# Performance work log

Measured on AMD Instinct MI355X. Metric: run time of the kernel, lower is better.

The kernel has to match this reference:

```python
import jax, jax.numpy as jnp
import numpy as np

ITEMNUM = 50000
NUM_HEADS = 4
EPS = 1e-8


def _ln(x, g, b):
    m = x.mean(-1, keepdims=True)
    v = ((x - m) ** 2).mean(-1, keepdims=True)
    return (x - m) * jax.lax.rsqrt(v + EPS) * g + b


def _forward(seqs_data, position, seqs, time_emb, pos_table, gate_W, gate_b,
             ln_attn_g, ln_attn_b, qW, qb, kW, kb, vW, vb,
             ln_ffn_g, ln_ffn_b, c1W, c1b, c2W, c2b, last_g, last_b):
    B, L, H = seqs.shape
    nb = qW.shape[0]
    hd = H // NUM_HEADS

    pe = pos_table[position]                      # [B,L,H]
    seqs = seqs + pe
    time = time_emb + pe
    # per-position per-block time gates, [B,L,nb]
    gates = jax.nn.sigmoid(jnp.einsum('blh,nh->bln', time, gate_W) + gate_b)

    keep = (seqs_data != ITEMNUM - 1)[..., None].astype(seqs.dtype)  # [B,L,1]
    seqs = seqs * keep
    tril = jnp.tril(jnp.ones((L, L), dtype=bool))  # causal: keep lower triangle
    neg_inf = jnp.asarray(-jnp.inf, seqs.dtype)
    scale = 1.0 / np.sqrt(hd).astype(np.float32)

    for i in range(nb):
        Q = _ln(seqs, ln_attn_g[i], ln_attn_b[i])
        q = Q @ qW[i].T + qb[i]
        k = time @ kW[i].T + kb[i]
        v = (seqs + time) @ vW[i].T + vb[i]
        # [B,nh,L,hd]
        q = q.reshape(B, L, NUM_HEADS, hd).transpose(0, 2, 1, 3)
        k = k.reshape(B, L, NUM_HEADS, hd).transpose(0, 2, 1, 3)
        v = v.reshape(B, L, NUM_HEADS, hd).transpose(0, 2, 1, 3)
        scores = jnp.einsum('bhqd,bhkd->bhqk', q, k) * scale  # [B,nh,L,L]
        tg = gates[:, :, i]                                   # [B,L]
        gate_mat = tg[:, None, :, None] * tg[:, None, None, :]  # [B,1,L,L] outer product
        scores = jnp.where(tril[None, None], scores * gate_mat, neg_inf)
        attn = jax.nn.softmax(scores, axis=-1)
        out = jnp.einsum('bhqk,bhkd->bhqd', attn, v)
        out = out.transpose(0, 2, 1, 3).reshape(B, L, H)
        x = Q + out
        x = _ln(x, ln_ffn_g[i], ln_ffn_b[i])
        # PointWiseFeedForward: two 1x1 convs == two linears, relu, residual
        h = jax.nn.relu(x @ c1W[i].T + c1b[i])
        seqs = (h @ c2W[i].T + c2b[i] + x) * keep

    return _ln(seqs, last_g, last_b)


def setup_inputs() -> dict:
    key = jax.random.key(0)
    B, L, H, NB, ML = 64, 512, 256, 2, 512
    ks = iter(jax.random.split(key, 32))
    nrm = lambda shape, s=0.05: jax.random.normal(next(ks), shape, jnp.float32) * s
    pos_table = nrm((ML, H), 0.02).at[0].set(0.0)  # padding_idx=0
    inp = {
        'seqs_data': jax.random.randint(next(ks), (B, L), 0, ITEMNUM - 1, jnp.int32),
        'seqs': nrm((B, L, H), 1.0),
        'position': jax.random.randint(next(ks), (B, L), 0, ML, jnp.int32),
        'time_emb': nrm((B, L, H), 1.0),
        'pos_table': pos_table,
        'gate_W': nrm((NB, H)), 'gate_b': jnp.zeros((NB,), jnp.float32),
        'ln_attn_g': jnp.ones((NB, H), jnp.float32), 'ln_attn_b': jnp.zeros((NB, H), jnp.float32),
        'qW': nrm((NB, H, H)), 'qb': jnp.zeros((NB, H), jnp.float32),
        'kW': nrm((NB, H, H)), 'kb': jnp.zeros((NB, H), jnp.float32),
        'vW': nrm((NB, H, H)), 'vb': jnp.zeros((NB, H), jnp.float32),
        'ln_ffn_g': jnp.ones((NB, H), jnp.float32), 'ln_ffn_b': jnp.zeros((NB, H), jnp.float32),
        'c1W': nrm((NB, H, H)), 'c1b': jnp.zeros((NB, H), jnp.float32),
        'c2W': nrm((NB, H, H)), 'c2b': jnp.zeros((NB, H), jnp.float32),
        'last_g': jnp.ones((H,), jnp.float32), 'last_b': jnp.zeros((H,), jnp.float32),
    }
    return inp


def reference(seqs_data, seqs, position, time_emb, pos_table, gate_W, gate_b,
              ln_attn_g, ln_attn_b, qW, qb, kW, kb, vW, vb,
              ln_ffn_g, ln_ffn_b, c1W, c1b, c2W, c2b, last_g, last_b):
    return _forward(seqs_data, position, seqs, time_emb, pos_table, gate_W, gate_b,
                    ln_attn_g, ln_attn_b, qW, qb, kW, kb, vW, vb,
                    ln_ffn_g, ln_ffn_b, c1W, c1b, c2W, c2b, last_g, last_b)
```

## Files before the change

### kernel.cpp

```cpp
#include <hip/hip_runtime.h>
#include <hip/hip_bf16.h>
#include <math.h>

#define NTOK 32768
#define Hdim 256
#define Ldim 512
#define Bdim 64
#define NHEAD 4
#define HD 64
#define PADV 49999

typedef __bf16 bf16x8 __attribute__((ext_vector_type(8)));
typedef __bf16 bf16x4 __attribute__((ext_vector_type(4)));
typedef float  f32x4  __attribute__((ext_vector_type(4)));

union bf8u { bf16x8 v8; bf16x4 v4[2]; };

__device__ __forceinline__ unsigned short f2bf(float f) {
    unsigned int u = __float_as_uint(f);
    unsigned int r = (u + 0x7fffu + ((u >> 16) & 1u)) >> 16;
    return (unsigned short)r;
}
__device__ __forceinline__ float bf2f(unsigned short u) {
    return __uint_as_float(((unsigned int)u) << 16);
}

__device__ __forceinline__ void gload16(const void* g, void* l) {
    __builtin_amdgcn_global_load_lds((const __attribute__((address_space(1))) unsigned int*)g,
                                     (__attribute__((address_space(3))) unsigned int*)l,
                                     16, 0, 0);
}

__global__ __launch_bounds__(256)
void castw_kernel(const float* __restrict__ q, const float* __restrict__ k,
                  const float* __restrict__ v, const float* __restrict__ c1,
                  const float* __restrict__ c2, unsigned short* __restrict__ dst) {
    const float* srcs[5] = {q, k, v, c1, c2};
    const float* s = srcs[blockIdx.y];
    int idx = blockIdx.x * 1024 + threadIdx.x * 4;
    float4 f = *(const float4*)(s + idx);
    unsigned short* d = dst + (size_t)blockIdx.y * 131072 + idx;
    d[0] = f2bf(f.x); d[1] = f2bf(f.y); d[2] = f2bf(f.z); d[3] = f2bf(f.w);
}

__global__ __launch_bounds__(256)
void prep_ln_kernel(const int* __restrict__ seqs_data, const float* __restrict__ seqs,
                    const int* __restrict__ position, const float* __restrict__ time_emb,
                    const float* __restrict__ pos_table, const float* __restrict__ gate_W,
                    const float* __restrict__ gate_b,
                    const float* __restrict__ lnG, const float* __restrict__ lnB,
                    unsigned short* __restrict__ Tbf,
                    unsigned short* __restrict__ QXbf,
                    unsigned short* __restrict__ VINbf,
                    float* __restrict__ gates, float* __restrict__ keepv) {
    int tok  = blockIdx.x * 4 + (threadIdx.x >> 6);
    int lane = threadIdx.x & 63;
    size_t off = (size_t)tok * Hdim + lane * 4;
    int pos = position[tok];
    float4 pe = *(const float4*)(pos_table + (size_t)pos * Hdim + lane * 4);
    float4 sq = *(const float4*)(seqs + off);
    float4 tm = *(const float4*)(time_emb + off);
    float keep = (seqs_data[tok] != PADV) ? 1.0f : 0.0f;
    float4 t = {tm.x + pe.x, tm.y + pe.y, tm.z + pe.z, tm.w + pe.w};
    float4 s = {(sq.x + pe.x) * keep, (sq.y + pe.y) * keep,
                (sq.z + pe.z) * keep, (sq.w + pe.w) * keep};
    ushort4 tb = {f2bf(t.x), f2bf(t.y), f2bf(t.z), f2bf(t.w)};
    *(ushort4*)(Tbf + off) = tb;
    float4 gw0 = *(const float4*)(gate_W + lane * 4);
    float4 gw1 = *(const float4*)(gate_W + Hdim + lane * 4);
    float r0 = s.x + s.y + s.z + s.w;
    float r1 = s.x * s.x + s.y * s.y + s.z * s.z + s.w * s.w;
    float r2 = t.x * gw0.x + t.y * gw0.y + t.z * gw0.z + t.w * gw0.w;
    float r3 = t.x * gw1.x + t.y * gw1.y + t.z * gw1.z + t.w * gw1.w;
#pragma unroll
    for (int o = 1; o < 64; o <<= 1) {
        r0 += __shfl_xor(r0, o, 64);
        r1 += __shfl_xor(r1, o, 64);
        r2 += __shfl_xor(r2, o, 64);
        r3 += __shfl_xor(r3, o, 64);
    }
    float mean = r0 * (1.0f / Hdim);
    float var  = fmaxf(r1 * (1.0f / Hdim) - mean * mean, 0.0f);
    float rstd = rsqrtf(var + 1e-8f);
    if (lane == 0) {
        gates[(size_t)tok * 2 + 0] = 1.0f / (1.0f + __expf(-(r2 + gate_b[0])));
        gates[(size_t)tok * 2 + 1] = 1.0f / (1.0f + __expf(-(r3 + gate_b[1])));
        keepv[tok] = keep;
    }
    float4 g4 = *(const float4*)(lnG + lane * 4);
    float4 b4 = *(const float4*)(lnB + lane * 4);
    float4 y = {(s.x - mean) * rstd * g4.x + b4.x, (s.y - mean) * rstd * g4.y + b4.y,
                (s.z - mean) * rstd * g4.z + b4.z, (s.w - mean) * rstd * g4.w + b4.w};
    ushort4 yb = {f2bf(y.x), f2bf(y.y), f2bf(y.z), f2bf(y.w)};
    *(ushort4*)(QXbf + off) = yb;
    ushort4 vb = {f2bf(s.x + t.x), f2bf(s.y + t.y), f2bf(s.z + t.z), f2bf(s.w + t.w)};
    *(ushort4*)(VINbf + off) = vb;
}

__global__ __launch_bounds__(256)
void ln2_kernel(unsigned short* QXbf, const unsigned short* __restrict__ QA,
                const float* __restrict__ lnG, const float* __restrict__ lnB) {
    int tok  = blockIdx.x * 4 + (threadIdx.x >> 6);
    int lane = threadIdx.x & 63;
    size_t off = (size_t)tok * Hdim + lane * 4;
    ushort4 q = *(const ushort4*)(QXbf + off);
    ushort4 a = *(const ushort4*)(QA + off);
    float4 x = {bf2f(q.x) + bf2f(a.x), bf2f(q.y) + bf2f(a.y),
                bf2f(q.z) + bf2f(a.z), bf2f(q.w) + bf2f(a.w)};
    float r0 = x.x + x.y + x.z + x.w;
    float r1 = x.x * x.x + x.y * x.y + x.z * x.z + x.w * x.w;
#pragma unroll
    for (int o = 1; o < 64; o <<= 1) {
        r0 += __shfl_xor(r0, o, 64);
        r1 += __shfl_xor(r1, o, 64);
    }
    float mean = r0 * (1.0f / Hdim);
    float var  = fmaxf(r1 * (1.0f / Hdim) - mean * mean, 0.0f);
    float rstd = rsqrtf(var + 1e-8f);
    float4 g4 = *(const float4*)(lnG + lane * 4);
    float4 b4 = *(const float4*)(lnB + lane * 4);
    ushort4 yb = {f2bf((x.x - mean) * rstd * g4.x + b4.x),
                  f2bf((x.y - mean) * rstd * g4.y + b4.y),
                  f2bf((x.z - mean) * rstd * g4.z + b4.z),
                  f2bf((x.w - mean) * rstd * g4.w + b4.w)};
    *(ushort4*)(QXbf + off) = yb;
}

__global__ __launch_bounds__(256)
void lnout_kernel(const unsigned short* __restrict__ Zbf,
                  unsigned short* QXbf,
                  const unsigned short* __restrict__ Tbf,
                  const float* __restrict__ keepv,
                  const float* __restrict__ lnG, const float* __restrict__ lnB,
                  float* __restrict__ outF,
                  unsigned short* __restrict__ outVIN) {
    int tok  = blockIdx.x * 4 + (threadIdx.x >> 6);
    int lane = threadIdx.x & 63;
    size_t off = (size_t)tok * Hdim + lane * 4;
    ushort4 z = *(const ushort4*)(Zbf + off);
    ushort4 x = *(const ushort4*)(QXbf + off);
    float kf = keepv[tok];
    float4 s = {(bf2f(z.x) + bf2f(x.x)) * kf, (bf2f(z.y) + bf2f(x.y)) * kf,
                (bf2f(z.z) + bf2f(x.z)) * kf, (bf2f(z.w) + bf2f(x.w)) * kf};
    float r0 = s.x + s.y + s.z + s.w;
    float r1 = s.x * s.x + s.y * s.y + s.z * s.z + s.w * s.w;
#pragma unroll
    for (int o = 1; o < 64; o <<= 1) {
        r0 += __shfl_xor(r0, o, 64);
        r1 += __shfl_xor(r1, o, 64);
    }
    float mean = r0 * (1.0f / Hdim);
    float var  = fmaxf(r1 * (1.0f / Hdim) - mean * mean, 0.0f);
    float rstd = rsqrtf(var + 1e-8f);
    float4 g4 = *(const float4*)(lnG + lane * 4);
    float4 b4 = *(const float4*)(lnB + lane * 4);
    float4 y = {(s.x - mean) * rstd * g4.x + b4.x, (s.y - mean) * rstd * g4.y + b4.y,
                (s.z - mean) * rstd * g4.z + b4.z, (s.w - mean) * rstd * g4.w + b4.w};
    if (outF) {
        *(float4*)(outF + off) = y;
    } else {
        ushort4 yb = {f2bf(y.x), f2bf(y.y), f2bf(y.z), f2bf(y.w)};
        *(ushort4*)(QXbf + off) = yb;
        ushort4 t = *(const ushort4*)(Tbf + off);
        ushort4 vb = {f2bf(s.x + bf2f(t.x)), f2bf(s.y + bf2f(t.y)),
                      f2bf(s.z + bf2f(t.z)), f2bf(s.w + bf2f(t.w))};
        *(ushort4*)(outVIN + off) = vb;
    }
}

#define GBM 128
#define GBN 128
#define GBK 64

__device__ __forceinline__ void stage64(const unsigned short* __restrict__ src,
                                        size_t rowBase, __bf16* lds, int tid, int kc) {
#pragma unroll
    for (int it = 0; it < 4; ++it) {
        int c = tid + it * 256;
        int r = c >> 3, sub = c & 7;
        int g = sub ^ (r & 7);
        gload16(src + (rowBase + r) * Hdim + kc + g * 8, lds + c * 8);
    }
}
__device__ __forceinline__ bf16x8 frag64(const __bf16* lds, int r, int g) {
    return *(const bf16x8*)(lds + r * 64 + (g ^ (r & 7)) * 8);
}

__global__ __launch_bounds__(256)
void gemm_qkv_kernel(const unsigned short* __restrict__ QXbf,
                     const unsigned short* __restrict__ Tbf,
                     const unsigned short* __restrict__ VINbf,
                     const unsigned short* __restrict__ qW,
                     const unsigned short* __restrict__ kW,
                     const unsigned short* __restrict__ vW,
                     const float* __restrict__ qb, const float* __restrict__ kb,
                     const float* __restrict__ vb,
                     unsigned short* __restrict__ Qbf,
                     unsigned short* __restrict__ Kbf,
                     unsigned short* __restrict__ VT) {
    __shared__ __align__(16) char smem[128 * 136 * 2];
    __bf16* As = (__bf16*)smem;
    __bf16* Ws = (__bf16*)(smem + 16384);
    __bf16 (*Ct)[136] = (__bf16 (*)[136])smem;
    int z = blockIdx.z;
    const unsigned short* A = (z == 0) ? QXbf : (z == 1) ? Tbf : VINbf;
    const unsigned short* W = (z == 0) ? qW : (z == 1) ? kW : vW;
    const float* bias       = (z == 0) ? qb : (z == 1) ? kb : vb;

    int tid = threadIdx.x, lane = tid & 63, w = tid >> 6;
    int wr = w >> 1, wc = w & 1;
    int m0 = blockIdx.y * GBM, n0 = blockIdx.x * GBN;
    f32x4 acc[4][4];
#pragma unroll
    for (int i = 0; i < 4; ++i)
#pragma unroll
        for (int j = 0; j < 4; ++j) acc[i][j] = (f32x4)(0.0f);
    int colq = lane & 15, kg = lane >> 4;
    for (int kc = 0; kc < Hdim; kc += GBK) {
        __syncthreads();
        stage64(A, m0, As, tid, kc);
        stage64(W, n0, Ws, tid, kc);
        __syncthreads();
        bf16x8 af[4][2], bfr[4][2];
#pragma unroll
        for (int i = 0; i < 4; ++i) {
            int r = wr * 64 + i * 16 + colq;
            af[i][0] = frag64(As, r, kg);
            af[i][1] = frag64(As, r, 4 + kg);
        }
#pragma unroll
        for (int j = 0; j < 4; ++j) {
            int r = wc * 64 + j * 16 + colq;
            bfr[j][0] = frag64(Ws, r, kg);
            bfr[j][1] = frag64(Ws, r, 4 + kg);
        }
#pragma unroll
        for (int i = 0; i < 4; ++i)
#pragma unroll
            for (int j = 0; j < 4; ++j) {
                acc[i][j] = __builtin_amdgcn_mfma_f32_16x16x32_bf16(af[i][0], bfr[j][0], acc[i][j], 0, 0, 0);
                acc[i][j] = __builtin_amdgcn_mfma_f32_16x16x32_bf16(af[i][1], bfr[j][1], acc[i][j], 0, 0, 0);
            }
    }
    int rowq = (lane >> 4) * 4;
    if (z < 2) {
        unsigned short* outBF = (z == 0) ? Qbf : Kbf;
#pragma unroll
        for (int i = 0; i < 4; ++i)
#pragma unroll
            for (int r = 0; r < 4; ++r) {
                int m = m0 + wr * 64 + i * 16 + rowq + r;
#pragma unroll
                for (int j = 0; j < 4; ++j) {
                    int n = n0 + wc * 64 + j * 16 + colq;
                    outBF[(size_t)m * Hdim + n] = f2bf(acc[i][j][r] + bias[n]);
                }
            }
    } else {
        __syncthreads();
#pragma unroll
        for (int i = 0; i < 4; ++i)
#pragma unroll
            for (int r = 0; r < 4; ++r) {
                int ml = wr * 64 + i * 16 + rowq + r;
#pragma unroll
                for (int j = 0; j < 4; ++j) {
                    int nl = wc * 64 + j * 16 + colq;
                    Ct[nl][ml] = (__bf16)(acc[i][j][r] + bias[n0 + nl]);
                }
            }
        __syncthreads();
        int bb = m0 >> 9, l0 = m0 & 511;
#pragma unroll
        for (int it = 0; it < 8; ++it) {
            int c = tid + it * 256;
            int nl = c >> 4;
            int o8 = (c & 15) * 8;
            int n = n0 + nl;
            int hh = n >> 6, dd = n & 63;
            bf16x8 v = *(const bf16x8*)&Ct[nl][o8];
            *(bf16x8*)(VT + ((((size_t)bb * NHEAD + hh) * HD + dd) * Ldim + l0 + o8)) = v;
        }
    }
}

__global__ __launch_bounds__(256)
void gemm_plain_kernel(const unsigned short* __restrict__ A,
                       const unsigned short* __restrict__ W,
                       const float* __restrict__ bias,
                       unsigned short* __restrict__ outBF, int doRelu) {
    __shared__ __align__(16) __bf16 As[128 * 64];
    __shared__ __align__(16) __bf16 Ws[128 * 64];
    int tid = threadIdx.x, lane = tid & 63, w = tid >> 6;
    int wr = w >> 1, wc = w & 1;
    int m0 = blockIdx.y * GBM, n0 = blockIdx.x * GBN;
    f32x4 acc[4][4];
#pragma unroll
    for (int i = 0; i < 4; ++i)
#pragma unroll
        for (int j = 0; j < 4; ++j) acc[i][j] = (f32x4)(0.0f);
    int colq = lane & 15, kg = lane >> 4;
    for (int kc = 0; kc < Hdim; kc += GBK) {
        __syncthreads();
        stage64(A, m0, As, tid, kc);
        stage64(W, n0, Ws, tid, kc);
        __syncthreads();
        bf16x8 af[4][2], bfr[4][2];
#pragma unroll
        for (int i = 0; i < 4; ++i) {
            int r = wr * 64 + i * 16 + colq;
            af[i][0] = frag64(As, r, kg);
            af[i][1] = frag64(As, r, 4 + kg);
        }
#pragma unroll
        for (int j = 0; j < 4; ++j) {
            int r = wc * 64 + j * 16 + colq;
            bfr[j][0] = frag64(Ws, r, kg);
            bfr[j][1] = frag64(Ws, r, 4 + kg);
        }
#pragma unroll
        for (int i = 0; i < 4; ++i)
#pragma unroll
            for (int j = 0; j < 4; ++j) {
                acc[i][j] = __builtin_amdgcn_mfma_f32_16x16x32_bf16(af[i][0], bfr[j][0], acc[i][j], 0, 0, 0);
                acc[i][j] = __builtin_amdgcn_mfma_f32_16x16x32_bf16(af[i][1], bfr[j][1], acc[i][j], 0, 0, 0);
            }
    }
    int rowq = (lane >> 4) * 4;
#pragma unroll
    for (int i = 0; i < 4; ++i)
#pragma unroll
        for (int r = 0; r < 4; ++r) {
            int m = m0 + wr * 64 + i * 16 + rowq + r;
#pragma unroll
            for (int j = 0; j < 4; ++j) {
                int n = n0 + wc * 64 + j * 16 + colq;
                float v = acc[i][j][r] + bias[n];
                if (doRelu) v = fmaxf(v, 0.0f);
                outBF[(size_t)m * Hdim + n] = f2bf(v);
            }
        }
}

#define AKS 68
#define AVS 516
#define APS 68
#define ATTN_LDS (512 * AKS * 2 + 64 * AVS * 2 + 192 * APS * 2)
__global__ __launch_bounds__(768, 1)
void attn_mfma_kernel(const unsigned short* __restrict__ Qg,
                      const unsigned short* __restrict__ Kg,
                      const unsigned short* __restrict__ VTg,
                      const float* __restrict__ gates,
                      unsigned short* __restrict__ Ob, int blk) {
    extern __shared__ __align__(16) char smem[];
    __bf16 (*Ks)[AKS]  = (__bf16 (*)[AKS])smem;
    __bf16 (*VTs)[AVS] = (__bf16 (*)[AVS])(smem + 512 * AKS * 2);
    __bf16 (*Ps)[APS]  = (__bf16 (*)[APS])(smem + 512 * AKS * 2 + 64 * AVS * 2);
    int h = blockIdx.x & 3, b = blockIdx.x >> 2;
    int tid = threadIdx.x, lane = tid & 63, w = tid >> 6;
    int colq = lane & 15, grp = lane >> 4;
    int rowq = grp * 4, kq = grp * 8;

    size_t baseK = (size_t)b * Ldim * Hdim + h * HD;
    for (int c = tid; c < 4096; c += 768) {
        int r = c >> 3, o = (c & 7) * 8;
        bf8u u;
        u.v8 = *(const bf16x8*)(Kg + baseK + (size_t)r * Hdim + o);
        *(bf16x4*)&Ks[r][o]     = u.v4[0];
        *(bf16x4*)&Ks[r][o + 4] = u.v4[1];
    }
    size_t baseV = ((size_t)b * NHEAD + h) * HD * Ldim;
    for (int c = tid; c < 4096; c += 768) {
        int d = c >> 6, k = (c & 63) * 8;
        bf8u u;
        u.v8 = *(const bf16x8*)(VTg + baseV + (size_t)d * Ldim + k);
        *(bf16x4*)&VTs[d][k]     = u.v4[0];
        *(bf16x4*)&VTs[d][k + 4] = u.v4[1];
    }
    __syncthreads();

    const float lscale = 0.125f * 1.44269504f;
    int gl[3], ng;
    if (w < 4)      { gl[0] = w;     gl[1] = 8 + w;  gl[2] = 28 + w; ng = 3; }
    else if (w < 8) { gl[0] = w;     gl[1] = 8 + w;  gl[2] = 16 + w; ng = 3; }
    else            { gl[0] = 8 + w; gl[1] = 16 + w; gl[2] = 0;      ng = 2; }

    for (int gi = 0; gi < ng; ++gi) {
        int g = gl[gi];
        int q0 = g * 16;
        size_t qrow = (size_t)(b * Ldim + q0 + colq) * Hdim + h * HD;
        bf16x8 afq0 = *(const bf16x8*)(Qg + qrow + kq);
        bf16x8 afq1 = *(const bf16x8*)(Qg + qrow + 32 + kq);
        float gql[4];
#pragma unroll
        for (int r = 0; r < 4; ++r)
            gql[r] = gates[((size_t)b * Ldim + q0 + rowq + r) * 2 + blk] * lscale;

        float lrun[4] = {0.0f, 0.0f, 0.0f, 0.0f};
        f32x4 accO[4];
#pragma unroll
        for (int jd = 0; jd < 4; ++jd) accO[jd] = (f32x4)(0.0f);

        int nfull = g >> 2;
        for (int kt = 0; kt <= nfull; ++kt) {
            int k0 = kt * 64;
            bool diag = (kt == nfull);
            f32x4 sv[4];
#pragma unroll
            for (int j = 0; j < 4; ++j) sv[j] = (f32x4)(0.0f);
#pragma unroll
            for (int j = 0; j < 4; ++j) {
                int kr = k0 + j * 16 + colq;
                bf8u b0, b1;
                b0.v4[0] = *(const bf16x4*)&Ks[kr][kq];
                b0.v4[1] = *(const bf16x4*)&Ks[kr][kq + 4];
                b1.v4[0] = *(const bf16x4*)&Ks[kr][32 + kq];
                b1.v4[1] = *(const bf16x4*)&Ks[kr][32 + kq + 4];
                sv[j] = __builtin_amdgcn_mfma_f32_16x16x32_bf16(afq0, b0.v8, sv[j], 0, 0, 0);
                sv[j] = __builtin_amdgcn_mfma_f32_16x16x32_bf16(afq1, b1.v8, sv[j], 0, 0, 0);
            }
            float gkv[4];
#pragma unroll
            for (int j = 0; j < 4; ++j)
                gkv[j] = gates[((size_t)b * Ldim + k0 + j * 16 + colq) * 2 + blk];
#pragma unroll
            for (int r = 0; r < 4; ++r) {
                float su = 0.0f;
                float p4[4];
                if (diag) {
                    int qg = q0 + rowq + r;
#pragma unroll
                    for (int j = 0; j < 4; ++j) {
                        float v = sv[j][r] * gql[r] * gkv[j];
                        v = (k0 + j * 16 + colq > qg) ? -1e38f : v;
                        float e = exp2f(v);
                        p4[j] = e;
                        su += e;
                    }
                } else {
#pragma unroll
                    for (int j = 0; j < 4; ++j) {
                        float e = exp2f(sv[j][r] * gql[r] * gkv[j]);
                        p4[j] = e;
                        su += e;
                    }
                }
#pragma unroll
                for (int off = 1; off < 16; off <<= 1)
                    su += __shfl_xor(su, off, 16);
                lrun[r] += su;
#pragma unroll
                for (int j = 0; j < 4; ++j)
                    Ps[w * 16 + rowq + r][j * 16 + colq] = (__bf16)p4[j];
            }
            bf8u a0, a1;
            a0.v4[0] = *(const bf16x4*)&Ps[w * 16 + colq][kq];
            a0.v4[1] = *(const bf16x4*)&Ps[w * 16 + colq][kq + 4];
            a1.v4[0] = *(const bf16x4*)&Ps[w * 16 + colq][32 + kq];
            a1.v4[1] = *(const bf16x4*)&Ps[w * 16 + colq][32 + kq + 4];
#pragma unroll
            for (int jd = 0; jd < 4; ++jd) {
                int vr = jd * 16 + colq;
                bf8u v0, v1;
                v0.v4[0] = *(const bf16x4*)&VTs[vr][k0 + kq];
                v0.v4[1] = *(const bf16x4*)&VTs[vr][k0 + kq + 4];
                v1.v4[0] = *(const bf16x4*)&VTs[vr][k0 + 32 + kq];
                v1.v4[1] = *(const bf16x4*)&VTs[vr][k0 + 32 + kq + 4];
                accO[jd] = __builtin_amdgcn_mfma_f32_16x16x32_bf16(a0.v8, v0.v8, accO[jd], 0, 0, 0);
                accO[jd] = __builtin_amdgcn_mfma_f32_16x16x32_bf16(a1.v8, v1.v8, accO[jd], 0, 0, 0);
            }
        }
#pragma unroll
        for (int r = 0; r < 4; ++r) {
            float inv = 1.0f / lrun[r];
#pragma unroll
            for (int jd = 0; jd < 4; ++jd)
                Ob[(size_t)(b * Ldim + q0 + rowq + r) * Hdim + h * HD + jd * 16 + colq] =
                    f2bf(accO[jd][r] * inv);
        }
    }
}

extern "C" void kernel_launch(void* const* d_in, const int* in_sizes, int n_in,
                              void* d_out, int out_size, void* d_ws, size_t ws_size,
                              hipStream_t stream) {
    const int*   seqs_data = (const int*)d_in[0];
    const float* seqs      = (const float*)d_in[1];
    const int*   position  = (const int*)d_in[2];
    const float* time_emb  = (const float*)d_in[3];
    const float* pos_table = (const float*)d_in[4];
    const float* gate_W    = (const float*)d_in[5];
    const float* gate_b    = (const float*)d_in[6];
    const float* ln_attn_g = (const float*)d_in[7];
    const float* ln_attn_b = (const float*)d_in[8];
    const float* qW        = (const float*)d_in[9];
    const float* qb        = (const float*)d_in[10];
    const float* kW        = (const float*)d_in[11];
    const float* kb        = (const float*)d_in[12];
    const float* vW        = (const float*)d_in[13];
    const float* vb        = (const float*)d_in[14];
    const float* ln_ffn_g  = (const float*)d_in[15];
    const float* ln_ffn_b  = (const float*)d_in[16];
    const float* c1W       = (const float*)d_in[17];
    const float* c1b       = (const float*)d_in[18];
    const float* c2W       = (const float*)d_in[19];
    const float* c2b       = (const float*)d_in[20];
    const float* last_g    = (const float*)d_in[21];
    const float* last_b    = (const float*)d_in[22];

    size_t BUF = (size_t)NTOK * Hdim;
    float* fws = (float*)d_ws;
    float* GATES = fws;
    float* KEEP  = GATES + (size_t)NTOK * 2;
    unsigned short* bws   = (unsigned short*)(KEEP + NTOK);
    unsigned short* Tbf   = bws;
    unsigned short* QXbf  = Tbf + BUF;
    unsigned short* VINbf = QXbf + BUF;
    unsigned short* HIDbf = VINbf + BUF;
    unsigned short* Qbf   = HIDbf + BUF;
    unsigned short* Kbf   = Qbf + BUF;
    unsigned short* VTbf  = Kbf + BUF;
    unsigned short* QAbf  = VTbf + BUF;
    unsigned short* Zbf   = QAbf + BUF;
    unsigned short* Wbf   = Zbf + BUF;
    size_t WB = (size_t)Hdim * Hdim;
    unsigned short* qWbf  = Wbf;
    unsigned short* kWbf  = Wbf + 2 * WB;
    unsigned short* vWbf  = Wbf + 4 * WB;
    unsigned short* c1Wbf = Wbf + 6 * WB;
    unsigned short* c2Wbf = Wbf + 8 * WB;

    castw_kernel<<<dim3(128, 5), 256, 0, stream>>>(qW, kW, vW, c1W, c2W, Wbf);
    prep_ln_kernel<<<NTOK / 4, 256, 0, stream>>>(seqs_data, seqs, position, time_emb,
                                                 pos_table, gate_W, gate_b,
                                                 ln_attn_g, ln_attn_b,
                                                 Tbf, QXbf, VINbf, GATES, KEEP);

    dim3 qkvgrid(Hdim / GBN, NTOK / GBM, 3);
    dim3 ggrid(Hdim / GBN, NTOK / GBM);
    for (int i = 0; i < 2; ++i) {
        gemm_qkv_kernel<<<qkvgrid, 256, 0, stream>>>(QXbf, Tbf, VINbf,
                                                     qWbf + i * WB, kWbf + i * WB, vWbf + i * WB,
                                                     qb + i * Hdim, kb + i * Hdim, vb + i * Hdim,
                                                     Qbf, Kbf, VTbf);
        attn_mfma_kernel<<<Bdim * NHEAD, 768, ATTN_LDS, stream>>>(Qbf, Kbf, VTbf, GATES, QAbf, i);
        ln2_kernel<<<NTOK / 4, 256, 0, stream>>>(QXbf, QAbf,
                                                 ln_ffn_g + i * Hdim, ln_ffn_b + i * Hdim);
        gemm_plain_kernel<<<ggrid, 256, 0, stream>>>(QXbf, c1Wbf + i * WB, c1b + i * Hdim, HIDbf, 1);
        gemm_plain_kernel<<<ggrid, 256, 0, stream>>>(HIDbf, c2Wbf + i * WB, c2b + i * Hdim, Zbf, 0);
        if (i == 0) {
            lnout_kernel<<<NTOK / 4, 256, 0, stream>>>(
                Zbf, QXbf, Tbf, KEEP,
                ln_attn_g + Hdim, ln_attn_b + Hdim,
                nullptr, VINbf);
        } else {
            lnout_kernel<<<NTOK / 4, 256, 0, stream>>>(
                Zbf, QXbf, Tbf, KEEP,
                last_g, last_b,
                (float*)d_out, nullptr);
        }
    }
}
```

Before: 378.2 us.

## Fuse post-attention LayerNorm, both FFN GEMMs and output LayerNorm into one kernel

Replaces ln2_kernel, the two gemm_plain launches and lnout_kernel with a single ffn_kernel. Each 512-thread block owns 128 tokens and keeps the normalized activations and the hidden layer in 64 KB of LDS across both GEMMs, streaming only the weights. This removes the global round trips for the LN output, the hidden activations and Z, plus three launches per block. In exchange there are only 256 blocks at one block per CU, with heavy register use (xc, sc and xnreg arrays) and weight tiles reloaded by every block.

Result: faster. 354.1 us (-6.4%).

```diff
diff --git a/kernel.cpp b/kernel.cpp
--- a/kernel.cpp
+++ b/kernel.cpp
@@ -13,6 +13,7 @@
 typedef __bf16 bf16x8 __attribute__((ext_vector_type(8)));
 typedef __bf16 bf16x4 __attribute__((ext_vector_type(4)));
 typedef float  f32x4  __attribute__((ext_vector_type(4)));
+typedef unsigned short u16x8 __attribute__((ext_vector_type(8)));
 
 union bf8u { bf16x8 v8; bf16x4 v4[2]; };
 
@@ -97,77 +98,6 @@
     *(ushort4*)(VINbf + off) = vb;
 }
 
-__global__ __launch_bounds__(256)
-void ln2_kernel(unsigned short* QXbf, const unsigned short* __restrict__ QA,
-                const float* __restrict__ lnG, const float* __restrict__ lnB) {
-    int tok  = blockIdx.x * 4 + (threadIdx.x >> 6);
-    int lane = threadIdx.x & 63;
-    size_t off = (size_t)tok * Hdim + lane * 4;
-    ushort4 q = *(const ushort4*)(QXbf + off);
-    ushort4 a = *(const ushort4*)(QA + off);
-    float4 x = {bf2f(q.x) + bf2f(a.x), bf2f(q.y) + bf2f(a.y),
-                bf2f(q.z) + bf2f(a.z), bf2f(q.w) + bf2f(a.w)};
-    float r0 = x.x + x.y + x.z + x.w;
-    float r1 = x.x * x.x + x.y * x.y + x.z * x.z + x.w * x.w;
-#pragma unroll
-    for (int o = 1; o < 64; o <<= 1) {
-        r0 += __shfl_xor(r0, o, 64);
-        r1 += __shfl_xor(r1, o, 64);
-    }
-    float mean = r0 * (1.0f / Hdim);
-    float var  = fmaxf(r1 * (1.0f / Hdim) - mean * mean, 0.0f);
-    float rstd = rsqrtf(var + 1e-8f);
-    float4 g4 = *(const float4*)(lnG + lane * 4);
-    float4 b4 = *(const float4*)(lnB + lane * 4);
-    ushort4 yb = {f2bf((x.x - mean) * rstd * g4.x + b4.x),
-                  f2bf((x.y - mean) * rstd * g4.y + b4.y),
-                  f2bf((x.z - mean) * rstd * g4.z + b4.z),
-                  f2bf((x.w - mean) * rstd * g4.w + b4.w)};
-    *(ushort4*)(QXbf + off) = yb;
-}
-
-__global__ __launch_bounds__(256)
-void lnout_kernel(const unsigned short* __restrict__ Zbf,
-                  unsigned short* QXbf,
-                  const unsigned short* __restrict__ Tbf,
-                  const float* __restrict__ keepv,
-                  const float* __restrict__ lnG, const float* __restrict__ lnB,
-                  float* __restrict__ outF,
-                  unsigned short* __restrict__ outVIN) {
-    int tok  = blockIdx.x * 4 + (threadIdx.x >> 6);
-    int lane = threadIdx.x & 63;
-    size_t off = (size_t)tok * Hdim + lane * 4;
-    ushort4 z = *(const ushort4*)(Zbf + off);
-    ushort4 x = *(const ushort4*)(QXbf + off);
-    float kf = keepv[tok];
-    float4 s = {(bf2f(z.x) + bf2f(x.x)) * kf, (bf2f(z.y) + bf2f(x.y)) * kf,
-                (bf2f(z.z) + bf2f(x.z)) * kf, (bf2f(z.w) + bf2f(x.w)) * kf};
-    float r0 = s.x + s.y + s.z + s.w;
-    float r1 = s.x * s.x + s.y * s.y + s.z * s.z + s.w * s.w;
-#pragma unroll
-    for (int o = 1; o < 64; o <<= 1) {
-        r0 += __shfl_xor(r0, o, 64);
-        r1 += __shfl_xor(r1, o, 64);
-    }
-    float mean = r0 * (1.0f / Hdim);
-    float var  = fmaxf(r1 * (1.0f / Hdim) - mean * mean, 0.0f);
-    float rstd = rsqrtf(var + 1e-8f);
-    float4 g4 = *(const float4*)(lnG + lane * 4);
-    float4 b4 = *(const float4*)(lnB + lane * 4);
-    float4 y = {(s.x - mean) * rstd * g4.x + b4.x, (s.y - mean) * rstd * g4.y + b4.y,
-                (s.z - mean) * rstd * g4.z + b4.z, (s.w - mean) * rstd * g4.w + b4.w};
-    if (outF) {
-        *(float4*)(outF + off) = y;
-    } else {
-        ushort4 yb = {f2bf(y.x), f2bf(y.y), f2bf(y.z), f2bf(y.w)};
-        *(ushort4*)(QXbf + off) = yb;
-        ushort4 t = *(const ushort4*)(Tbf + off);
-        ushort4 vb = {f2bf(s.x + bf2f(t.x)), f2bf(s.y + bf2f(t.y)),
-                      f2bf(s.z + bf2f(t.z)), f2bf(s.w + bf2f(t.w))};
-        *(ushort4*)(outVIN + off) = vb;
-    }
-}
-
 #define GBM 128
 #define GBN 128
 #define GBK 64
@@ -284,39 +214,42 @@
     }
 }
 
-__global__ __launch_bounds__(256)
-void gemm_plain_kernel(const unsigned short* __restrict__ A,
-                       const unsigned short* __restrict__ W,
-                       const float* __restrict__ bias,
-                       unsigned short* __restrict__ outBF, int doRelu) {
-    __shared__ __align__(16) __bf16 As[128 * 64];
-    __shared__ __align__(16) __bf16 Ws[128 * 64];
-    int tid = threadIdx.x, lane = tid & 63, w = tid >> 6;
-    int wr = w >> 1, wc = w & 1;
-    int m0 = blockIdx.y * GBM, n0 = blockIdx.x * GBN;
-    f32x4 acc[4][4];
+#define FFN_LDS (65536 + 32768)
+
+__device__ __forceinline__ int swz(int r, int g) {
+    return (g & 24) | ((g & 7) ^ (r & 7));
+}
+
+__device__ __forceinline__ void ffn_gemm(const unsigned short* __restrict__ W,
+                                         const __bf16* Abuf, __bf16* Wst,
+                                         int tid, int wr, int wc, int colq, int kg,
+                                         f32x4 acc[4][4]) {
 #pragma unroll
     for (int i = 0; i < 4; ++i)
 #pragma unroll
         for (int j = 0; j < 4; ++j) acc[i][j] = (f32x4)(0.0f);
-    int colq = lane & 15, kg = lane >> 4;
-    for (int kc = 0; kc < Hdim; kc += GBK) {
+    for (int kc = 0; kc < Hdim; kc += 64) {
         __syncthreads();
-        stage64(A, m0, As, tid, kc);
-        stage64(W, n0, Ws, tid, kc);
+#pragma unroll
+        for (int it = 0; it < 4; ++it) {
+            int c = tid + it * 512;
+            int r = c >> 3, sub = c & 7;
+            int g = sub ^ (r & 7);
+            gload16(W + (size_t)r * Hdim + kc + g * 8, Wst + c * 8);
+        }
         __syncthreads();
         bf16x8 af[4][2], bfr[4][2];
 #pragma unroll
         for (int i = 0; i < 4; ++i) {
             int r = wr * 64 + i * 16 + colq;
-            af[i][0] = frag64(As, r, kg);
-            af[i][1] = frag64(As, r, 4 + kg);
+            af[i][0] = *(const bf16x8*)(Abuf + r * 256 + kc + ((kg) ^ (r & 7)) * 8);
+            af[i][1] = *(const bf16x8*)(Abuf + r * 256 + kc + ((4 + kg) ^ (r & 7)) * 8);
         }
 #pragma unroll
         for (int j = 0; j < 4; ++j) {
-            int r = wc * 64 + j * 16 + colq;
-            bfr[j][0] = frag64(Ws, r, kg);
-            bfr[j][1] = frag64(Ws, r, 4 + kg);
+            int n = wc * 64 + j * 16 + colq;
+            bfr[j][0] = frag64(Wst, n, kg);
+            bfr[j][1] = frag64(Wst, n, 4 + kg);
         }
 #pragma unroll
         for (int i = 0; i < 4; ++i)
@@ -326,20 +259,166 @@
                 acc[i][j] = __builtin_amdgcn_mfma_f32_16x16x32_bf16(af[i][1], bfr[j][1], acc[i][j], 0, 0, 0);
             }
     }
+}
+
+__global__ __launch_bounds__(512, 1)
+void ffn_kernel(const unsigned short* __restrict__ Qx,
+                const unsigned short* __restrict__ Qa,
+                const float* __restrict__ lnG, const float* __restrict__ lnB,
+                const unsigned short* __restrict__ c1Wb, const float* __restrict__ c1b,
+                const unsigned short* __restrict__ c2Wb, const float* __restrict__ c2b,
+                const float* __restrict__ keepv,
+                const unsigned short* __restrict__ Tbf,
+                const float* __restrict__ oG, const float* __restrict__ oB,
+                float* __restrict__ outF,
+                unsigned short* __restrict__ QxOut,
+                unsigned short* __restrict__ VINout) {
+    extern __shared__ __align__(16) char smem[];
+    __bf16* Abuf   = (__bf16*)smem;
+    __bf16* Wst    = (__bf16*)(smem + 65536);
+    float*  statsF = (float*)(smem + 65536);
+
+    int m0  = blockIdx.x * 128;
+    int tid = threadIdx.x, lane = tid & 63, w = tid >> 6;
+    int wr = w >> 2, wc = w & 3;
+    int colq = lane & 15, kg = lane >> 4;
     int rowq = (lane >> 4) * 4;
+
+    float xc[8][8];
+#pragma unroll
+    for (int it = 0; it < 8; ++it) {
+        int c = tid + it * 512;
+        int r = c >> 5, g = c & 31;
+        size_t off = (size_t)(m0 + r) * Hdim + g * 8;
+        u16x8 qv = *(const u16x8*)(Qx + off);
+        u16x8 av = *(const u16x8*)(Qa + off);
+        float cs = 0.0f, cq = 0.0f;
+#pragma unroll
+        for (int j = 0; j < 8; ++j) {
+            float x = bf2f(qv[j]) + bf2f(av[j]);
+            xc[it][j] = x;
+            cs += x; cq += x * x;
+        }
+#pragma unroll
+        for (int o = 1; o < 32; o <<= 1) {
+            cs += __shfl_xor(cs, o, 32);
+            cq += __shfl_xor(cq, o, 32);
+        }
+        if ((tid & 31) == 0) { statsF[r * 2] = cs; statsF[r * 2 + 1] = cq; }
+    }
+    __syncthreads();
+    u16x8 xnreg[8];
+#pragma unroll
+    for (int it = 0; it < 8; ++it) {
+        int c = tid + it * 512;
+        int r = c >> 5, g = c & 31, col = g * 8;
+        float mean = statsF[r * 2] * (1.0f / Hdim);
+        float var  = fmaxf(statsF[r * 2 + 1] * (1.0f / Hdim) - mean * mean, 0.0f);
+        float rstd = rsqrtf(var + 1e-8f);
+        float4 g0 = *(const float4*)(lnG + col), g1 = *(const float4*)(lnG + col + 4);
+        float4 b0 = *(const float4*)(lnB + col), b1 = *(const float4*)(lnB + col + 4);
+        float gv[8] = {g0.x, g0.y, g0.z, g0.w, g1.x, g1.y, g1.z, g1.w};
+        float bv[8] = {b0.x, b0.y, b0.z, b0.w, b1.x, b1.y, b1.z, b1.w};
+        u16x8 xn;
+#pragma unroll
+        for (int j = 0; j < 8; ++j)
+            xn[j] = f2bf((xc[it][j] - mean) * rstd * gv[j] + bv[j]);
+        xnreg[it] = xn;
+        *(u16x8*)(Abuf + r * 256 + swz(r, g) * 8) = xn;
+    }
+
+    f32x4 acc[4][4];
+    ffn_gemm(c1Wb, Abuf, Wst, tid, wr, wc, colq, kg, acc);
+    float bj[4];
+#pragma unroll
+    for (int j = 0; j < 4; ++j) bj[j] = c1b[wc * 64 + j * 16 + colq];
+    __syncthreads();
 #pragma unroll
     for (int i = 0; i < 4; ++i)
 #pragma unroll
         for (int r = 0; r < 4; ++r) {
-            int m = m0 + wr * 64 + i * 16 + rowq + r;
+            int m = wr * 64 + i * 16 + rowq + r;
 #pragma unroll
             for (int j = 0; j < 4; ++j) {
-                int n = n0 + wc * 64 + j * 16 + colq;
-                float v = acc[i][j][r] + bias[n];
-                if (doRelu) v = fmaxf(v, 0.0f);
-                outBF[(size_t)m * Hdim + n] = f2bf(v);
-            }
-        }
+                int n = wc * 64 + j * 16 + colq;
+                float v = fmaxf(acc[i][j][r] + bj[j], 0.0f);
+                Abuf[m * 256 + swz(m, n >> 3) * 8 + (n & 7)] = (__bf16)v;
+            }
+        }
+
+    ffn_gemm(c2Wb, Abuf, Wst, tid, wr, wc, colq, kg, acc);
+#pragma unroll
+    for (int j = 0; j < 4; ++j) bj[j] = c2b[wc * 64 + j * 16 + colq];
+    __syncthreads();
+#pragma unroll
+    for (int i = 0; i < 4; ++i)
+#pragma unroll
+        for (int r = 0; r < 4; ++r) {
+            int m = wr * 64 + i * 16 + rowq + r;
+#pragma unroll
+            for (int j = 0; j < 4; ++j) {
+                int n = wc * 64 + j * 16 + colq;
+                Abuf[m * 256 + swz(m, n >> 3) * 8 + (n & 7)] = (__bf16)(acc[i][j][r] + bj[j]);
+            }
+        }
+    __syncthreads();
+
+    float sc[8][8];
+#pragma unroll
+    for (int it = 0; it < 8; ++it) {
+        int c = tid + it * 512;
+        int r = c >> 5, g = c & 31;
+        u16x8 zv = *(const u16x8*)(Abuf + r * 256 + swz(r, g) * 8);
+        u16x8 xn = xnreg[it];
+        float kf = keepv[m0 + r];
+        float cs = 0.0f, cq = 0.0f;
+#pragma unroll
+        for (int j = 0; j < 8; ++j) {
+            float s = (bf2f(zv[j]) + bf2f(xn[j])) * kf;
+            sc[it][j] = s;
+            cs += s; cq += s * s;
+        }
+#pragma unroll
+        for (int o = 1; o < 32; o <<= 1) {
+            cs += __shfl_xor(cs, o, 32);
+            cq += __shfl_xor(cq, o, 32);
+        }
+        if ((tid & 31) == 0) { statsF[r * 2] = cs; statsF[r * 2 + 1] = cq; }
+    }
+    __syncthreads();
+#pragma unroll
+    for (int it = 0; it < 8; ++it) {
+        int c = tid + it * 512;
+        int r = c >> 5, g = c & 31, col = g * 8;
+        float mean = statsF[r * 2] * (1.0f / Hdim);
+        float var  = fmaxf(statsF[r * 2 + 1] * (1.0f / Hdim) - mean * mean, 0.0f);
+        float rstd = rsqrtf(var + 1e-8f);
+        float4 g0 = *(const float4*)(oG + col), g1 = *(const float4*)(oG + col + 4);
+        float4 b0 = *(const float4*)(oB + col), b1 = *(const float4*)(oB + col + 4);
+        float gv[8] = {g0.x, g0.y, g0.z, g0.w, g1.x, g1.y, g1.z, g1.w};
+        float bv[8] = {b0.x, b0.y, b0.z, b0.w, b1.x, b1.y, b1.z, b1.w};
+        size_t off = (size_t)(m0 + r) * Hdim + col;
+        float y[8];
+#pragma unroll
+        for (int j = 0; j < 8; ++j)
+            y[j] = (sc[it][j] - mean) * rstd * gv[j] + bv[j];
+        if (outF) {
+            float4 o0 = {y[0], y[1], y[2], y[3]};
+            float4 o1 = {y[4], y[5], y[6], y[7]};
+            *(float4*)(outF + off)     = o0;
+            *(float4*)(outF + off + 4) = o1;
+        } else {
+            u16x8 yb, vb;
+            u16x8 tv = *(const u16x8*)(Tbf + off);
+#pragma unroll
+            for (int j = 0; j < 8; ++j) {
+                yb[j] = f2bf(y[j]);
+                vb[j] = f2bf(sc[it][j] + bf2f(tv[j]));
+            }
+            *(u16x8*)(QxOut + off)  = yb;
+            *(u16x8*)(VINout + off) = vb;
+        }
+    }
 }
 
 #define AKS 68
@@ -537,27 +616,21 @@
                                                  Tbf, QXbf, VINbf, GATES, KEEP);
 
     dim3 qkvgrid(Hdim / GBN, NTOK / GBM, 3);
-    dim3 ggrid(Hdim / GBN, NTOK / GBM);
     for (int i = 0; i < 2; ++i) {
         gemm_qkv_kernel<<<qkvgrid, 256, 0, stream>>>(QXbf, Tbf, VINbf,
                                                      qWbf + i * WB, kWbf + i * WB, vWbf + i * WB,
                                                      qb + i * Hdim, kb + i * Hdim, vb + i * Hdim,
                                                      Qbf, Kbf, VTbf);
         attn_mfma_kernel<<<Bdim * NHEAD, 768, ATTN_LDS, stream>>>(Qbf, Kbf, VTbf, GATES, QAbf, i);
-        ln2_kernel<<<NTOK / 4, 256, 0, stream>>>(QXbf, QAbf,
-                                                 ln_ffn_g + i * Hdim, ln_ffn_b + i * Hdim);
-        gemm_plain_kernel<<<ggrid, 256, 0, stream>>>(QXbf, c1Wbf + i * WB, c1b + i * Hdim, HIDbf, 1);
-        gemm_plain_kernel<<<ggrid, 256, 0, stream>>>(HIDbf, c2Wbf + i * WB, c2b + i * Hdim, Zbf, 0);
-        if (i == 0) {
-            lnout_kernel<<<NTOK / 4, 256, 0, stream>>>(
-                Zbf, QXbf, Tbf, KEEP,
-                ln_attn_g + Hdim, ln_attn_b + Hdim,
-                nullptr, VINbf);
-        } else {
-            lnout_kernel<<<NTOK / 4, 256, 0, stream>>>(
-                Zbf, QXbf, Tbf, KEEP,
-                last_g, last_b,
-                (float*)d_out, nullptr);
-        }
-    }
-}
+        ffn_kernel<<<NTOK / 128, 512, FFN_LDS, stream>>>(
+            QXbf, QAbf,
+            ln_ffn_g + i * Hdim, ln_ffn_b + i * Hdim,
+            c1Wbf + i * WB, c1b + i * Hdim,
+            c2Wbf + i * WB, c2b + i * Hdim,
+            KEEP, Tbf,
+            (i == 0) ? ln_attn_g + Hdim : last_g,
+            (i == 0) ? ln_attn_b + Hdim : last_b,
+            (i == 0) ? nullptr : (float*)d_out,
+            QXbf, VINbf);
+    }
+}
```
